# Optimization experiments

Measured on AMD Instinct MI355X. Metric: run time of the kernel, lower is better.

## Reference

```python
import jax, jax.numpy as jnp
import numpy as np

VERY_NEGATIVE_NUMBER = -1e30


def setup_inputs() -> dict:
    key = jax.random.key(0)
    ks = jax.random.split(key, 7)
    B, N, M, D = 16, 1024, 1024, 128
    inv_sqrt_d = 1.0 / np.sqrt(D).astype(np.float32)
    query = jax.random.normal(ks[0], (B, N, D), jnp.float32)
    memory = jax.random.normal(ks[1], (B, M, D), jnp.float32)
    # trilinear similarity parameters (BiDAF)
    w_q = jax.random.normal(ks[2], (D,), jnp.float32) * inv_sqrt_d
    w_m = jax.random.normal(ks[3], (D,), jnp.float32) * inv_sqrt_d
    w_qm = jax.random.normal(ks[4], (D,), jnp.float32) * inv_sqrt_d
    query_mask = jax.random.randint(ks[5], (B, N), 0, 2, jnp.int32)
    memory_mask = jax.random.randint(ks[6], (B, M), 0, 2, jnp.int32)
    return {
        "query": query,
        "memory": memory,
        "w_q": w_q,
        "w_m": w_m,
        "w_qm": w_qm,
        "query_mask": query_mask,
        "memory_mask": memory_mask,
    }


def reference(query, memory, w_q, w_m, w_qm, query_mask, memory_mask):
    # trilinear similarity: sim[b,n,m] = w_q.q_n + w_m.m_m + sum_d w_qm_d * q_nd * m_md
    sim = (
        jnp.einsum("bnd,d->bn", query, w_q)[:, :, None]
        + jnp.einsum("bmd,d->bm", memory, w_m)[:, None, :]
        + jnp.einsum("bnd,d,bmd->bnm", query, w_qm, memory)
    )  # [B, N, M]
    mask = (
        query_mask[:, :, None].astype(sim.dtype)
        * memory_mask[:, None, :].astype(sim.dtype)
    )  # [B, N, M]
    sim = sim + (1.0 - mask) * VERY_NEGATIVE_NUMBER
    # query -> memory attention (row-wise softmax over memory axis)
    q2m_prob = jax.nn.softmax(sim, axis=-1)  # [B, N, M]
    query_memory_attention = jnp.einsum("bnm,bmd->bnd", q2m_prob, memory)
    # memory -> query attention (softmax over row maxima, one vector per batch)
    m2q_prob = jax.nn.softmax(jnp.max(sim, axis=-1), axis=-1)  # [B, N]
    m2q = jnp.einsum("bn,bnd->bd", m2q_prob, query)[:, None, :]  # [B, 1, D]
    memory_query_attention = jnp.broadcast_to(m2q, query_memory_attention.shape)
    return (query_memory_attention, memory_query_attention)
```

## Files before the change

### kernel.cpp

```cpp
#include <hip/hip_runtime.h>
#include <hip/hip_bf16.h>
#include <stdint.h>

#define BB 16
#define NN 1024
#define MM 1024
#define DD 128
#define VERY_NEG (-1e30f)
#define LOG2E 1.44269504f
#define NCHUNK 16

using bf16x8 = __attribute__((ext_vector_type(8))) short;
using f32x4  = __attribute__((ext_vector_type(4))) float;

__device__ inline unsigned short f2bf(float f) {
    union { float f; uint32_t u; } cv; cv.f = f;
    uint32_t u = cv.u;
    return (unsigned short)((u + 0x7FFFu + ((u >> 16) & 1u)) >> 16);
}
#define EXP2F(x) __builtin_amdgcn_exp2f(x)

typedef __attribute__((address_space(3))) unsigned int lds_u32;
typedef const __attribute__((address_space(1))) unsigned int glb_u32;
__device__ __forceinline__ void gl16(const void* g, void* l) {
    __builtin_amdgcn_global_load_lds((glb_u32*)g, (lds_u32*)l, 16, 0, 0);
}

__global__ void prep_rows(const float* __restrict__ q, const float* __restrict__ mem,
                          const float* __restrict__ wq, const float* __restrict__ wm,
                          const float* __restrict__ wqm, const int* __restrict__ mmask,
                          float* __restrict__ a, float* __restrict__ c1s,
                          unsigned short* __restrict__ qp, unsigned short* __restrict__ mb)
{
    int wave = (blockIdx.x * 256 + threadIdx.x) >> 6;
    int lane = threadIdx.x & 63;
    bool is_q = wave < BB * NN;
    int row = is_q ? wave : wave - BB * NN;
    const float* src = (is_q ? q : mem) + (size_t)row * DD;
    const float* wd  = is_q ? wq : wm;
    float2 v  = *(const float2*)(src + lane * 2);
    float2 w2 = *(const float2*)(wd + lane * 2);
    float dot = v.x * w2.x + v.y * w2.y;
    #pragma unroll
    for (int o = 32; o; o >>= 1) dot += __shfl_xor(dot, o);
    if (lane == 0) {
        if (is_q) a[row] = dot;
        else {
            int mm = mmask[row];
            c1s[row] = (dot + (mm ? 0.f : VERY_NEG)) * LOG2E;
        }
    }
    float2 s2 = v;
    if (is_q) {
        float2 wv = *(const float2*)(wqm + lane * 2);
        s2.x *= wv.x * LOG2E; s2.y *= wv.y * LOG2E;
    }
    ushort2 o2; o2.x = f2bf(s2.x); o2.y = f2bf(s2.y);
    *(ushort2*)((is_q ? qp : mb) + (size_t)row * DD + lane * 2) = o2;
}

__global__ void transpose_mem(const float* __restrict__ mem, unsigned short* __restrict__ mt)
{
    __shared__ unsigned short t[64][72];
    int bid = blockIdx.x;
    int dt = bid & 1, mtile = (bid >> 1) & 15, b = bid >> 5;
    int d0 = dt * 64, m0 = mtile * 64;
    int tid = threadIdx.x;
    int cc = tid & 63, rr = tid >> 6;
    #pragma unroll
    for (int r = 0; r < 64; r += 4) {
        float v = mem[((size_t)b * MM + m0 + r + rr) * DD + d0 + cc];
        t[cc][r + rr] = f2bf(v);
    }
    __syncthreads();
    #pragma unroll
    for (int r = 0; r < 64; r += 4) {
        mt[((size_t)b * DD + d0 + r + rr) * MM + m0 + cc] = t[r + rr][cc];
    }
}

__global__ __launch_bounds__(256) void flash_fwd(
    const unsigned short* __restrict__ qp, const unsigned short* __restrict__ mb,
    const unsigned short* __restrict__ mt,
    const float* __restrict__ a, const float* __restrict__ c1s,
    const int* __restrict__ qmask,
    float* __restrict__ out1, float* __restrict__ rowmax)
{
    __shared__ unsigned short Kb[2][8192];
    __shared__ unsigned short Vb[2][8192];
    __shared__ unsigned short pl[4][16][72];
    __shared__ float c1L[MM];

    int tid = threadIdx.x;
    int w = tid >> 6, lane = tid & 63;
    int g = lane >> 4, qi = lane & 15;
    int b = blockIdx.x >> 4, nt = blockIdx.x & 15;
    int n0q = nt * 64 + w * 16;

    const unsigned short* mbB = mb + (size_t)b * MM * DD;
    const unsigned short* mtB = mt + (size_t)b * DD * MM;

    {
        float4 cv = *(const float4*)(c1s + b * MM + tid * 4);
        *(float4*)&c1L[tid * 4] = cv;
    }

    const unsigned short* qpb = qp + ((size_t)b * NN + n0q) * DD;
    bf16x8 qf[4];
    #pragma unroll
    for (int kc = 0; kc < 4; kc++)
        qf[kc] = *(const bf16x8*)(qpb + qi * DD + kc * 32 + g * 8);

    float a_q = a[b * NN + n0q + qi];
    int   qm  = qmask[b * NN + n0q + qi];

    float m_run = -INFINITY, l_run = 0.f;
    f32x4 o[8];
    #pragma unroll
    for (int d2 = 0; d2 < 8; d2++) o[d2] = (f32x4){0.f, 0.f, 0.f, 0.f};

    auto stage = [&](int m0, unsigned short* Kc, unsigned short* Vc) {
        #pragma unroll
        for (int i = 0; i < 8; i++) {
            int j = w * 8 + i;
            if (j < 16) {
                const unsigned short* gsrc = mbB
                    + (size_t)(m0 + (j >> 2) * 16 + (lane & 15)) * DD
                    + (j & 3) * 32 + (lane >> 4) * 8;
                gl16(gsrc, Kc + j * 512);
            } else {
                int j2 = j - 16;
                const unsigned short* gsrc = mtB
                    + (size_t)((j2 >> 1) * 16 + (lane & 15)) * MM
                    + m0 + (j2 & 1) * 32 + (lane >> 4) * 8;
                gl16(gsrc, Vc + j2 * 512);
            }
        }
    };

    stage(0, Kb[0], Vb[0]);
    __syncthreads();

    int cur = 0;
    for (int ch = 0; ch < NCHUNK; ch++) {
        int m0 = ch * 64;
        if (ch + 1 < NCHUNK)
            stage(m0 + 64, Kb[cur ^ 1], Vb[cur ^ 1]);

        const unsigned short* Kc = Kb[cur];
        const unsigned short* Vc = Vb[cur];

        f32x4 st[4];
        #pragma unroll
        for (int t = 0; t < 4; t++) st[t] = (f32x4){0, 0, 0, 0};
        #pragma unroll
        for (int t = 0; t < 4; t++) {
            #pragma unroll
            for (int kc = 0; kc < 4; kc++) {
                bf16x8 af = *(const bf16x8*)(Kc + ((t * 4 + kc) * 64 + lane) * 8);
                st[t] = __builtin_amdgcn_mfma_f32_16x16x32_bf16(af, qf[kc], st[t], 0, 0, 0);
            }
        }
        float sv[4][4];
        float cmax = -INFINITY;
        #pragma unroll
        for (int t = 0; t < 4; t++) {
            float4 c1v = *(const float4*)&c1L[m0 + t * 16 + g * 4];
            float cc4[4] = {c1v.x, c1v.y, c1v.z, c1v.w};
            #pragma unroll
            for (int i = 0; i < 4; i++) {
                float s = qm ? (st[t][i] + cc4[i]) : 0.f;
                sv[t][i] = s;
                cmax = fmaxf(cmax, s);
            }
        }
        cmax = fmaxf(cmax, __shfl_xor(cmax, 16));
        cmax = fmaxf(cmax, __shfl_xor(cmax, 32));
        float m_new = fmaxf(m_run, cmax);
        float alpha = EXP2F(m_run - m_new);
        float psum = 0.f;
        #pragma unroll
        for (int t = 0; t < 4; t++) {
            unsigned short pe[4];
            #pragma unroll
            for (int i = 0; i < 4; i++) {
                float p = EXP2F(sv[t][i] - m_new);
                psum += p;
                pe[i] = f2bf(p);
            }
            ushort4 pw2; pw2.x = pe[0]; pw2.y = pe[1]; pw2.z = pe[2]; pw2.w = pe[3];
            *(ushort4*)(&pl[w][qi][t * 16 + g * 4]) = pw2;
        }
        psum += __shfl_xor(psum, 16);
        psum += __shfl_xor(psum, 32);
        l_run = l_run * alpha + psum;
        m_run = m_new;

        float aL[4];
        #pragma unroll
        for (int i = 0; i < 4; i++) aL[i] = __shfl(alpha, g * 4 + i);

        __builtin_amdgcn_sched_barrier(0);
        bf16x8 pa0 = *(const bf16x8*)(&pl[w][qi][g * 8]);
        bf16x8 pa1 = *(const bf16x8*)(&pl[w][qi][32 + g * 8]);
        #pragma unroll
        for (int d2 = 0; d2 < 8; d2++) {
            bf16x8 vf0 = *(const bf16x8*)(Vc + ((d2 * 2 + 0) * 64 + lane) * 8);
            bf16x8 vf1 = *(const bf16x8*)(Vc + ((d2 * 2 + 1) * 64 + lane) * 8);
            f32x4 oo = o[d2];
            #pragma unroll
            for (int i = 0; i < 4; i++) oo[i] *= aL[i];
            oo = __builtin_amdgcn_mfma_f32_16x16x32_bf16(pa0, vf0, oo, 0, 0, 0);
            o[d2] = __builtin_amdgcn_mfma_f32_16x16x32_bf16(pa1, vf1, oo, 0, 0, 0);
        }

        __syncthreads();
        cur ^= 1;
    }

    float inv[4];
    #pragma unroll
    for (int i = 0; i < 4; i++) inv[i] = 1.f / __shfl(l_run, g * 4 + i);
    #pragma unroll
    for (int d2 = 0; d2 < 8; d2++) {
        #pragma unroll
        for (int i = 0; i < 4; i++)
            out1[((size_t)b * NN + n0q + g * 4 + i) * DD + d2 * 16 + qi] = o[d2][i] * inv[i];
    }
    if (lane < 16)
        rowmax[b * NN + n0q + qi] = m_run * (1.f / LOG2E) + a_q + (qm ? 0.f : VERY_NEG);
}

__global__ __launch_bounds__(256) void m2q_partial(
    const float* __restrict__ rowmax, const float* __restrict__ query,
    float* __restrict__ partial, float* __restrict__ Zbuf)
{
    int bid = blockIdx.x;
    int b = bid >> 3, ch = bid & 7;
    int tid = threadIdx.x, lane = tid & 63, wv = tid >> 6;
    __shared__ float red[8];
    __shared__ float pe[128];
    __shared__ float acc1[128];

    float4 rv = *(const float4*)(rowmax + b * NN + tid * 4);
    float mx = fmaxf(fmaxf(rv.x, rv.y), fmaxf(rv.z, rv.w));
    #pragma unroll
    for (int o = 32; o; o >>= 1) mx = fmaxf(mx, __shfl_xor(mx, o));
    if (lane == 0) red[wv] = mx;
    __syncthreads();
    mx = fmaxf(fmaxf(red[0], red[1]), fmaxf(red[2], red[3]));
    float ls = __expf(rv.x - mx) + __expf(rv.y - mx) + __expf(rv.z - mx) + __expf(rv.w - mx);
    #pragma unroll
    for (int o = 32; o; o >>= 1) ls += __shfl_xor(ls, o);
    if (lane == 0) red[4 + wv] = ls;
    if (tid < 128) pe[tid] = __expf(rowmax[b * NN + ch * 128 + tid] - mx);
    __syncthreads();
    float Z = (red[4] + red[5]) + (red[6] + red[7]);

    int d = tid & 127, h = tid >> 7;
    const float* qb = query + ((size_t)b * NN + ch * 128 + h * 64) * DD + d;
    float acc = 0.f;
    #pragma unroll 8
    for (int n = 0; n < 64; n++) acc += pe[h * 64 + n] * qb[(size_t)n * DD];
    if (h) acc1[d] = acc;
    __syncthreads();
    if (!h) partial[(b * 8 + ch) * DD + d] = acc + acc1[d];
    if (tid == 0) Zbuf[b] = Z;
}

__global__ __launch_bounds__(256) void bcast_kernel(
    const float* __restrict__ partial, const float* __restrict__ Zbuf,
    float4* __restrict__ out2)
{
    __shared__ float m2qL[128];
    int i = blockIdx.x * 256 + threadIdx.x;
    int b = i >> 15;
    int tid = threadIdx.x;
    if (tid < 128) {
        float s = 0.f;
        #pragma unroll
        for (int ch = 0; ch < 8; ch++) s += partial[(b * 8 + ch) * DD + tid];
        m2qL[tid] = s / Zbuf[b];
    }
    __syncthreads();
    out2[i] = ((const float4*)m2qL)[i & 31];
}

extern "C" void kernel_launch(void* const* d_in, const int* in_sizes, int n_in,
                              void* d_out, int out_size, void* d_ws, size_t ws_size,
                              hipStream_t stream)
{
    const float* query  = (const float*)d_in[0];
    const float* memory = (const float*)d_in[1];
    const float* w_q    = (const float*)d_in[2];
    const float* w_m    = (const float*)d_in[3];
    const float* w_qm   = (const float*)d_in[4];
    const int*   qmask  = (const int*)d_in[5];
    const int*   mmask  = (const int*)d_in[6];
    float* out1 = (float*)d_out;
    float* out2 = out1 + (size_t)BB * NN * DD;

    char* ws = (char*)d_ws;
    float* a       = (float*)ws;
    float* c1s     = a + BB * NN;
    float* rowmax  = c1s + BB * MM;
    float* partial = rowmax + BB * NN;
    float* Zbuf    = partial + BB * 8 * DD;
    unsigned short* qp = (unsigned short*)(ws + (1 << 20));
    unsigned short* mb = qp + (size_t)BB * NN * DD;
    unsigned short* mt = mb + (size_t)BB * MM * DD;

    prep_rows<<<dim3((BB * NN + BB * MM) / 4), 256, 0, stream>>>(query, memory, w_q, w_m, w_qm, mmask, a, c1s, qp, mb);
    transpose_mem<<<dim3(BB * (MM / 64) * (DD / 64)), 256, 0, stream>>>(memory, mt);
    flash_fwd<<<dim3(BB * 16), 256, 0, stream>>>(qp, mb, mt, a, c1s, qmask, out1, rowmax);
    m2q_partial<<<dim3(BB * 8), 256, 0, stream>>>(rowmax, query, partial, Zbuf);
    bcast_kernel<<<dim3(2048), 256, 0, stream>>>(partial, Zbuf, (float4*)out2);
}
```

Measured before the change: 56.39 us.

## Split memory axis across two wave groups per block and merge softmax states

The flash kernel now launches 512 threads per block. Two groups of four waves each process half of the memory axis (8 chunks instead of 16) with their own double-buffered K/V tiles in a larger dynamic LDS region. At the end, the partial max, sum and output accumulators are merged through LDS, with the output buffer reusing the K region. The aim is to halve the serial chunk loop and raise wave occupancy on the 256-block grid. The cost is more LDS, which may limit residency, plus an extra reduction with two barriers.

```diff
diff --git a/kernel.cpp b/kernel.cpp
--- a/kernel.cpp
+++ b/kernel.cpp
@@ -8,7 +8,8 @@
 #define DD 128
 #define VERY_NEG (-1e30f)
 #define LOG2E 1.44269504f
-#define NCHUNK 16
+#define HALF_M 512
+#define NCH 8
 
 using bf16x8 = __attribute__((ext_vector_type(8))) short;
 using f32x4  = __attribute__((ext_vector_type(4))) float;
@@ -79,30 +80,34 @@
     }
 }
 
-__global__ __launch_bounds__(256) void flash_fwd(
+__global__ __launch_bounds__(512) void flash_fwd(
     const unsigned short* __restrict__ qp, const unsigned short* __restrict__ mb,
     const unsigned short* __restrict__ mt,
     const float* __restrict__ a, const float* __restrict__ c1s,
     const int* __restrict__ qmask,
     float* __restrict__ out1, float* __restrict__ rowmax)
 {
-    __shared__ unsigned short Kb[2][8192];
-    __shared__ unsigned short Vb[2][8192];
-    __shared__ unsigned short pl[4][16][72];
-    __shared__ float c1L[MM];
+    __shared__ __align__(16) char smem[155648];
+    unsigned short* KbBase = (unsigned short*)smem;
+    unsigned short* VbBase = (unsigned short*)(smem + 65536);
+    unsigned short (*pl)[16][72] = (unsigned short(*)[16][72])(smem + 131072);
+    float* c1L = (float*)(smem + 149504);
+    float (*mlb)[16][2] = (float(*)[16][2])(smem + 153600);
+    float (*Obuf)[16][130] = (float(*)[16][130])smem;
 
     int tid = threadIdx.x;
     int w = tid >> 6, lane = tid & 63;
+    int qt = w & 3, mh = w >> 2;
     int g = lane >> 4, qi = lane & 15;
     int b = blockIdx.x >> 4, nt = blockIdx.x & 15;
-    int n0q = nt * 64 + w * 16;
+    int n0q = nt * 64 + qt * 16;
 
     const unsigned short* mbB = mb + (size_t)b * MM * DD;
     const unsigned short* mtB = mt + (size_t)b * DD * MM;
 
     {
-        float4 cv = *(const float4*)(c1s + b * MM + tid * 4);
-        *(float4*)&c1L[tid * 4] = cv;
+        float2 cv = *(const float2*)(c1s + b * MM + tid * 2);
+        *(float2*)&c1L[tid * 2] = cv;
     }
 
     const unsigned short* qpb = qp + ((size_t)b * NN + n0q) * DD;
@@ -122,7 +127,7 @@
     auto stage = [&](int m0, unsigned short* Kc, unsigned short* Vc) {
         #pragma unroll
         for (int i = 0; i < 8; i++) {
-            int j = w * 8 + i;
+            int j = qt * 8 + i;
             if (j < 16) {
                 const unsigned short* gsrc = mbB
                     + (size_t)(m0 + (j >> 2) * 16 + (lane & 15)) * DD
@@ -137,18 +142,20 @@
             }
         }
     };
-
-    stage(0, Kb[0], Vb[0]);
+    auto Kbuf = [&](int bufi) { return KbBase + (mh * 2 + bufi) * 8192; };
+    auto Vbuf = [&](int bufi) { return VbBase + (mh * 2 + bufi) * 8192; };
+
+    stage(mh * HALF_M, Kbuf(0), Vbuf(0));
     __syncthreads();
 
     int cur = 0;
-    for (int ch = 0; ch < NCHUNK; ch++) {
-        int m0 = ch * 64;
-        if (ch + 1 < NCHUNK)
-            stage(m0 + 64, Kb[cur ^ 1], Vb[cur ^ 1]);
-
-        const unsigned short* Kc = Kb[cur];
-        const unsigned short* Vc = Vb[cur];
+    for (int ch = 0; ch < NCH; ch++) {
+        int m0 = mh * HALF_M + ch * 64;
+        if (ch + 1 < NCH)
+            stage(m0 + 64, Kbuf(cur ^ 1), Vbuf(cur ^ 1));
+
+        const unsigned short* Kc = Kbuf(cur);
+        const unsigned short* Vc = Vbuf(cur);
 
         f32x4 st[4];
         #pragma unroll
@@ -218,17 +225,47 @@
         cur ^= 1;
     }
 
-    float inv[4];
-    #pragma unroll
-    for (int i = 0; i < 4; i++) inv[i] = 1.f / __shfl(l_run, g * 4 + i);
-    #pragma unroll
-    for (int d2 = 0; d2 < 8; d2++) {
-        #pragma unroll
-        for (int i = 0; i < 4; i++)
-            out1[((size_t)b * NN + n0q + g * 4 + i) * DD + d2 * 16 + qi] = o[d2][i] * inv[i];
-    }
-    if (lane < 16)
-        rowmax[b * NN + n0q + qi] = m_run * (1.f / LOG2E) + a_q + (qm ? 0.f : VERY_NEG);
+    if (g == 0) { mlb[w][qi][0] = m_run; mlb[w][qi][1] = l_run; }
+    __syncthreads();
+    int pw = w ^ 4;
+    float mo[4], mp[4];
+    #pragma unroll
+    for (int i = 0; i < 4; i++) {
+        int r = g * 4 + i;
+        mo[i] = __shfl(m_run, r);
+        mp[i] = mlb[pw][r][0];
+    }
+    if (mh == 0) {
+        #pragma unroll
+        for (int i = 0; i < 4; i++) {
+            float M = fmaxf(mo[i], mp[i]);
+            float wsc = EXP2F(mo[i] - M);
+            #pragma unroll
+            for (int d2 = 0; d2 < 8; d2++)
+                Obuf[qt][g * 4 + i][d2 * 16 + qi] = o[d2][i] * wsc;
+        }
+    }
+    __syncthreads();
+    if (mh == 1) {
+        #pragma unroll
+        for (int i = 0; i < 4; i++) {
+            int r = g * 4 + i;
+            float M = fmaxf(mo[i], mp[i]);
+            float ws1 = EXP2F(mo[i] - M);
+            float lo = __shfl(l_run, r);
+            float lg = mlb[pw][r][1] * EXP2F(mp[i] - M) + lo * ws1;
+            float invl = 1.f / lg;
+            #pragma unroll
+            for (int d2 = 0; d2 < 8; d2++) {
+                float val = (Obuf[qt][r][d2 * 16 + qi] + o[d2][i] * ws1) * invl;
+                out1[((size_t)b * NN + n0q + r) * DD + d2 * 16 + qi] = val;
+            }
+        }
+        if (g == 0) {
+            float M = fmaxf(m_run, mlb[pw][qi][0]);
+            rowmax[b * NN + n0q + qi] = M * (1.f / LOG2E) + a_q + (qm ? 0.f : VERY_NEG);
+        }
+    }
 }
 
 __global__ __launch_bounds__(256) void m2q_partial(
@@ -312,7 +349,7 @@
 
     prep_rows<<<dim3((BB * NN + BB * MM) / 4), 256, 0, stream>>>(query, memory, w_q, w_m, w_qm, mmask, a, c1s, qp, mb);
     transpose_mem<<<dim3(BB * (MM / 64) * (DD / 64)), 256, 0, stream>>>(memory, mt);
-    flash_fwd<<<dim3(BB * 16), 256, 0, stream>>>(qp, mb, mt, a, c1s, qmask, out1, rowmax);
+    flash_fwd<<<dim3(BB * 16), 512, 0, stream>>>(qp, mb, mt, a, c1s, qmask, out1, rowmax);
     m2q_partial<<<dim3(BB * 8), 256, 0, stream>>>(rowmax, query, partial, Zbuf);
     bcast_kernel<<<dim3(2048), 256, 0, stream>>>(partial, Zbuf, (float4*)out2);
 }
```

After: 55.48 us. About the same (-1.6%).
